# Kernel optimization log

Hardware: AMD Instinct MI355X
Metric: run time of the kernel (lower is better)

## Reference

```python
import jax, jax.numpy as jnp
import numpy as np

B, N = 1, 512
CS, CZ = 384, 128
H, DQK, DV, PQK, PV = 12, 16, 16, 4, 8
EPS = 1e-8
SW = float(np.sqrt(1.0 / (3 * DQK)))            # scalar_weights
PW = float(np.sqrt(1.0 / (3 * PQK * 9.0 / 2)))  # point_weights
ZW = float(np.sqrt(1.0 / 3))                    # attention_2d_weights


def _lin(key, din, dout):
    return 0.02 * jax.random.normal(key, (din, dout), dtype=jnp.float32), jnp.zeros((dout,), dtype=jnp.float32)


def setup_inputs():
    key = jax.random.key(0)
    ks = jax.random.split(key, 16)
    Wsq, bsq = _lin(ks[0], CS, H * DQK)
    Wsk, bsk = _lin(ks[1], CS, H * DQK)
    Wsv, bsv = _lin(ks[2], CS, H * DV)
    Wsb, bsb = _lin(ks[3], CZ, H)
    Wpq, bpq = _lin(ks[4], CS, H * PQK * 3)
    Wpk, bpk = _lin(ks[5], CS, H * PQK * 3)
    Wpv, bpv = _lin(ks[6], CS, H * PV * 3)
    Wout, bout = _lin(ks[7], H * (DV + PV * 4 + CZ), CS)
    w_attn = 0.5 * jax.random.normal(ks[8], (3,), dtype=jnp.float32)  # attn_linear weight (1,3)
    b_attn = jnp.zeros((), dtype=jnp.float32)
    tpw = jnp.full((H,), float(np.log(np.e - 1.0)), dtype=jnp.float32)  # trainable_point_weight
    s = jax.random.normal(ks[9], (B, N, CS), dtype=jnp.float32)
    z = jax.random.normal(ks[10], (B, N, N, CZ), dtype=jnp.float32)
    rot = jax.random.normal(ks[11], (B, N, 3, 3), dtype=jnp.float32)
    tran = jax.random.normal(ks[12], (B, N, 3), dtype=jnp.float32)
    res_mask = jnp.ones((B, N), dtype=jnp.float32)
    return dict(s=s, z=z, rot=rot, tran=tran, res_mask=res_mask,
                Wsq=Wsq, bsq=bsq, Wsk=Wsk, bsk=bsk, Wsv=Wsv, bsv=bsv,
                Wsb=Wsb, bsb=bsb, Wpq=Wpq, bpq=bpq, Wpk=Wpk, bpk=bpk,
                Wpv=Wpv, bpv=bpv, w_attn=w_attn, b_attn=b_attn, tpw=tpw,
                Wout=Wout, bout=bout)


def _ipa(s, z, rot, tran, res_mask, Wsq, bsq, Wsk, bsk, Wsv, bsv, Wsb, bsb,
         Wpq, bpq, Wpk, bpk, Wpv, bpv, w_attn, b_attn, tpw, Wout, bout):
    b, n, _ = s.shape
    sq = (s @ Wsq + bsq).reshape(b, n, H, DQK)
    sk = (s @ Wsk + bsk).reshape(b, n, H, DQK)
    sv = (s @ Wsv + bsv).reshape(b, n, H, DV)
    sb = z @ Wsb + bsb  # [b, i, j, h] pair bias

    def to_global(W, bias, p):
        t = (s @ W + bias).reshape(b, n, H, p, 3)
        return jnp.einsum('bnxy,bnhpy->bnhpx', rot, t) + tran[:, :, None, None, :]

    pqg = to_global(Wpq, bpq, PQK)
    pkg = to_global(Wpk, bpk, PQK)
    pvg = to_global(Wpv, bpv, PV)

    diff = pqg[:, :, None] - pkg[:, None, :]          # [b, i, j, h, p, 3]
    sdist = jnp.sum(diff * diff, axis=(-1, -2))       # [b, i, j, h]

    attn_point = -0.5 * jax.nn.softplus(tpw) * sdist * PW
    attn_scalar = jnp.einsum('bihd,bjhd->bijh', sq * SW, sk)
    attn_pair = sb * ZW
    # attn_linear(stack([scalar, point, pair], -1)).squeeze(-1)
    logits = attn_scalar * w_attn[0] + attn_point * w_attn[1] + attn_pair * w_attn[2] + b_attn

    mask2d = res_mask[:, :, None] * res_mask[:, None, :]
    logits = jnp.where(mask2d[..., None] == 0, jnp.finfo(logits.dtype).min, logits)
    attn = jax.nn.softmax(logits, axis=2)             # softmax over j

    r_scalar = jnp.einsum('bijh,bjhd->bihd', attn, sv)
    r_pt_g = jnp.einsum('bijh,bjhpc->bihpc', attn, pvg)
    # rotate back to local frame: R^T (x - t)
    r_pt = jnp.einsum('biyx,bihpy->bihpx', rot, r_pt_g - tran[:, :, None, None, :])
    r_norm = jnp.sqrt(jnp.sum(r_pt * r_pt, axis=-1) + EPS)  # [b, i, h, p]
    r_pair = jnp.einsum('bijh,bijc->bihc', attn, z)

    cat = jnp.concatenate([r_scalar, r_pt.reshape(b, n, H, PV * 3), r_norm, r_pair], axis=-1)
    return cat.reshape(b, n, -1) @ Wout + bout


def reference(s, z, rot, tran, res_mask, Wsq, bsq, Wsk, bsk, Wsv, bsv, Wsb, bsb,
              Wpq, bpq, Wpk, bpk, Wpv, bpv, w_attn, b_attn, tpw, Wout, bout):
    return _ipa(s, z, rot, tran, res_mask, Wsq, bsq, Wsk, bsk, Wsv, bsv, Wsb, bsb,
                Wpq, bpq, Wpk, bpk, Wpv, bpv, w_attn, b_attn, tpw, Wout, bout)
```

## Files before the change

### kernel.cpp

```cpp
#include <hip/hip_runtime.h>
#include <hip/hip_bf16.h>
#include <math.h>

#define NN 512
#define CSD 384
#define CZ 128
#define HH 12
#define TMPW 1152
#define CATH 176
#define CATDIM 2112
#define NSPLIT 6
#define KSPL 352

#define SW 0.14433756729740643f
#define PW 0.13608276348795434f
#define ZW 0.57735026918962576f
#define NEG_INF -3.4028234663852886e38f

typedef float f32x4_t __attribute__((ext_vector_type(4)));
typedef short bf16x8_t __attribute__((ext_vector_type(8)));

union BFU { uint4 q; bf16x8_t v; ushort u[8]; };

static __device__ __forceinline__ ushort f2bf(float f) {
    __hip_bfloat16 h = __float2bfloat16(f);
    return *reinterpret_cast<ushort*>(&h);
}
static __device__ __forceinline__ float bf2f(ushort u) {
    unsigned int v = ((unsigned int)u) << 16;
    return __uint_as_float(v);
}

__global__ void proj_gemm_kernel(const float* __restrict__ s, const float* __restrict__ rot,
                                 const float* __restrict__ tran,
                                 const float* __restrict__ Wsq, const float* __restrict__ bsq,
                                 const float* __restrict__ Wsk, const float* __restrict__ bsk,
                                 const float* __restrict__ Wsv, const float* __restrict__ bsv,
                                 const float* __restrict__ Wpq, const float* __restrict__ bpq,
                                 const float* __restrict__ Wpk, const float* __restrict__ bpk,
                                 const float* __restrict__ Wpv, const float* __restrict__ bpv,
                                 float* __restrict__ tmp)
{
    int bx = blockIdx.x;
    int n0 = blockIdx.y * 32;
    int f0 = bx * 48;
    const float* W; const float* bb; int dout; int segstart;
    if (bx < 4)       { W = Wsq; bb = bsq; dout = 192; segstart = 0; }
    else if (bx < 8)  { W = Wsk; bb = bsk; dout = 192; segstart = 192; }
    else if (bx < 12) { W = Wsv; bb = bsv; dout = 192; segstart = 384; }
    else if (bx < 15) { W = Wpq; bb = bpq; dout = 144; segstart = 576; }
    else if (bx < 18) { W = Wpk; bb = bpk; dout = 144; segstart = 720; }
    else              { W = Wpv; bb = bpv; dout = 288; segstart = 864; }
    int colbase = f0 - segstart;

    __shared__ float St[32][34];
    __shared__ float Ws[32][49];
    int tid = threadIdx.x;
    int ty = tid >> 4, tx = tid & 15;
    float acc[2][3] = {{0,0,0},{0,0,0}};

    for (int k0 = 0; k0 < CSD; k0 += 32) {
        {
            int r = tid >> 3, c4 = (tid & 7) * 4;
            float4 v = *(const float4*)&s[(size_t)(n0 + r) * CSD + k0 + c4];
            St[c4 + 0][r] = v.x; St[c4 + 1][r] = v.y; St[c4 + 2][r] = v.z; St[c4 + 3][r] = v.w;
        }
        for (int e = tid; e < 1536; e += 256) {
            int r = e / 48, c = e % 48;
            Ws[r][c] = W[(size_t)(k0 + r) * dout + colbase + c];
        }
        __syncthreads();
        #pragma unroll
        for (int k = 0; k < 32; k++) {
            float2 a = *(const float2*)&St[k][ty * 2];
            float b0 = Ws[k][tx * 3], b1 = Ws[k][tx * 3 + 1], b2 = Ws[k][tx * 3 + 2];
            acc[0][0] += a.x * b0; acc[0][1] += a.x * b1; acc[0][2] += a.x * b2;
            acc[1][0] += a.y * b0; acc[1][1] += a.y * b1; acc[1][2] += a.y * b2;
        }
        __syncthreads();
    }
    float bv0 = bb[colbase + tx * 3], bv1 = bb[colbase + tx * 3 + 1], bv2 = bb[colbase + tx * 3 + 2];
    #pragma unroll
    for (int r = 0; r < 2; r++) {
        int n = n0 + ty * 2 + r;
        float v0 = acc[r][0] + bv0, v1 = acc[r][1] + bv1, v2 = acc[r][2] + bv2;
        float* o = tmp + (size_t)n * TMPW + f0 + tx * 3;
        if (bx >= 12) {
            const float* R = rot + n * 9;
            const float* T = tran + n * 3;
            float g0 = R[0] * v0 + R[1] * v1 + R[2] * v2 + T[0];
            float g1 = R[3] * v0 + R[4] * v1 + R[5] * v2 + T[1];
            float g2 = R[6] * v0 + R[7] * v1 + R[8] * v2 + T[2];
            o[0] = g0; o[1] = g1; o[2] = g2;
        } else {
            o[0] = v0; o[1] = v1; o[2] = v2;
        }
    }
}

__global__ void pairbias_mfma_kernel(const float* __restrict__ z, const float* __restrict__ Wsb,
                                     const float* __restrict__ watt, float* __restrict__ sbz)
{
    int tid = threadIdx.x;
    int w = tid >> 6, lane = tid & 63;
    int l16 = lane & 15, lhi = lane >> 4;
    float A2 = watt[2] * ZW;

    BFU breg[4];
    #pragma unroll
    for (int kk = 0; kk < 4; kk++) {
        #pragma unroll
        for (int e = 0; e < 8; e++) {
            int k = kk * 32 + lhi * 8 + e;
            float v = (l16 < HH) ? Wsb[k * HH + l16] * A2 : 0.f;
            breg[kk].u[e] = f2bf(v);
        }
    }

    #pragma unroll
    for (int t = 0; t < 4; t++) {
        size_t r0 = (size_t)blockIdx.x * 256 + (size_t)(t * 4 + w) * 16;
        const float* zrow = z + (r0 + l16) * CZ;
        f32x4_t acc = {0.f, 0.f, 0.f, 0.f};
        #pragma unroll
        for (int kk = 0; kk < 4; kk++) {
            int k0 = kk * 32 + lhi * 8;
            float4 f0 = *(const float4*)&zrow[k0];
            float4 f1 = *(const float4*)&zrow[k0 + 4];
            BFU a;
            a.u[0] = f2bf(f0.x); a.u[1] = f2bf(f0.y); a.u[2] = f2bf(f0.z); a.u[3] = f2bf(f0.w);
            a.u[4] = f2bf(f1.x); a.u[5] = f2bf(f1.y); a.u[6] = f2bf(f1.z); a.u[7] = f2bf(f1.w);
            acc = __builtin_amdgcn_mfma_f32_16x16x32_bf16(a.v, breg[kk].v, acc, 0, 0, 0);
        }
        if (l16 < HH) {
            #pragma unroll
            for (int r = 0; r < 4; r++)
                sbz[(r0 + lhi * 4 + r) * HH + l16] = acc[r];
        }
    }
}

__global__ void logits_softmax_rpair_kernel(const float* __restrict__ z,
                                            const float* __restrict__ sbz,
                                            const float* __restrict__ resm,
                                            const float* __restrict__ bsb,
                                            const float* __restrict__ watt,
                                            const float* __restrict__ batt,
                                            const float* __restrict__ tpw,
                                            const float* __restrict__ tmp,
                                            ushort* __restrict__ attn_bf,
                                            float* __restrict__ cat)
{
    int i = blockIdx.x;
    __shared__ float lt[NN * 17];
    __shared__ uint4 Pl[16 * 64];
    __shared__ float sqs[192];
    __shared__ float pqi[144];
    __shared__ float cpt[12];
    __shared__ float cb[12];
    int tid = threadIdx.x;
    float w0 = watt[0], w1 = watt[1], w2 = watt[2], ba = batt[0];
    float A2 = w2 * ZW;

    for (int k = tid; k < 192; k += 256) sqs[k] = tmp[(size_t)i * TMPW + k] * (SW * w0);
    if (tid < 144) pqi[tid] = tmp[(size_t)i * TMPW + 576 + tid];
    if (tid < 12) {
        cpt[tid] = -0.5f * log1pf(expf(tpw[tid])) * PW * w1;
        cb[tid]  = A2 * bsb[tid] + ba;
    }
    __syncthreads();

    int jg = tid >> 2, hg = tid & 3, h0 = hg * 3;
    float rmi = resm[i];
    const float* sbi = sbz + (size_t)i * NN * HH;

    #pragma unroll
    for (int rr = 0; rr < 8; rr++) {
        int j = jg + 64 * rr;
        float mj = rmi * resm[j];
        const float* sbr = &sbi[(size_t)j * HH + h0];
        float pb[3] = { sbr[0], sbr[1], sbr[2] };
        #pragma unroll
        for (int t = 0; t < 3; t++) {
            int h = h0 + t;
            const float4* skp = (const float4*)(tmp + (size_t)j * TMPW + 192 + h * 16);
            const float4* sqp = (const float4*)&sqs[h * 16];
            float d0 = 0.f;
            #pragma unroll
            for (int q = 0; q < 4; q++) {
                float4 kv = skp[q];
                float4 qv = sqp[q];
                d0 += qv.x * kv.x + qv.y * kv.y + qv.z * kv.z + qv.w * kv.w;
            }
            const float4* pkp = (const float4*)(tmp + (size_t)j * TMPW + 720 + h * 12);
            const float4* pqp = (const float4*)&pqi[h * 12];
            float sd = 0.f;
            #pragma unroll
            for (int q = 0; q < 3; q++) {
                float4 kv = pkp[q];
                float4 qv = pqp[q];
                float a = qv.x - kv.x, bb2 = qv.y - kv.y, cc = qv.z - kv.z, e = qv.w - kv.w;
                sd += a * a + bb2 * bb2 + cc * cc + e * e;
            }
            float lg = cb[h] + pb[t] + d0 + cpt[h] * sd;
            if (mj == 0.f) lg = NEG_INF;
            lt[j * 17 + h] = lg;
        }
    }
    __syncthreads();

    int wid = tid >> 6, lane = tid & 63;
    #pragma unroll
    for (int t = 0; t < 3; t++) {
        int h = wid * 3 + t;
        float v[8]; float m = -INFINITY;
        #pragma unroll
        for (int u = 0; u < 8; u++) { v[u] = lt[(lane + 64 * u) * 17 + h]; m = fmaxf(m, v[u]); }
        for (int off = 32; off; off >>= 1) m = fmaxf(m, __shfl_xor(m, off));
        float ssum = 0.f;
        #pragma unroll
        for (int u = 0; u < 8; u++) { v[u] = __expf(v[u] - m); ssum += v[u]; }
        for (int off = 32; off; off >>= 1) ssum += __shfl_xor(ssum, off);
        float inv = 1.f / ssum;
        #pragma unroll
        for (int u = 0; u < 8; u++) lt[(lane + 64 * u) * 17 + h] = v[u] * inv;
    }
    __syncthreads();

    ushort* ab = attn_bf + (size_t)i * HH * NN;
    #pragma unroll
    for (int u = 0; u < 4; u++) {
        int s2 = tid + 256 * u;
        int m = s2 >> 6, g = s2 & 63;
        BFU val;
        if (m < HH) {
            #pragma unroll
            for (int e = 0; e < 8; e++) val.u[e] = f2bf(lt[(g * 8 + e) * 17 + m]);
            *(uint4*)&ab[(size_t)m * NN + g * 8] = val.q;
        } else {
            val.q.x = 0; val.q.y = 0; val.q.z = 0; val.q.w = 0;
        }
        Pl[m * 64 + (g ^ (m & 7))] = val.q;
    }
    __syncthreads();

    int l16 = lane & 15, lhi = lane >> 4;
    int c0a = (wid * 2 + 0) * 16, c0b = (wid * 2 + 1) * 16;
    f32x4_t acc0 = {0.f, 0.f, 0.f, 0.f};
    f32x4_t acc1 = {0.f, 0.f, 0.f, 0.f};

    for (int kk = 0; kk < 16; kk++) {
        int gidx = kk * 4 + lhi;
        BFU au;
        au.q = Pl[l16 * 64 + (gidx ^ (l16 & 7))];
        const float* zb = z + ((size_t)i * NN + kk * 32 + lhi * 8) * CZ;
        BFU b0, b1;
        #pragma unroll
        for (int e = 0; e < 8; e++) {
            b0.u[e] = f2bf(zb[(size_t)e * CZ + c0a + l16]);
            b1.u[e] = f2bf(zb[(size_t)e * CZ + c0b + l16]);
        }
        acc0 = __builtin_amdgcn_mfma_f32_16x16x32_bf16(au.v, b0.v, acc0, 0, 0, 0);
        acc1 = __builtin_amdgcn_mfma_f32_16x16x32_bf16(au.v, b1.v, acc1, 0, 0, 0);
    }

    #pragma unroll
    for (int r = 0; r < 4; r++) {
        int h = lhi * 4 + r;
        if (h < HH) {
            float* cp = cat + (size_t)i * CATDIM + h * CATH + 48;
            cp[c0a + l16] = acc0[r];
            cp[c0b + l16] = acc1[r];
        }
    }
}

__global__ void head_sum_kernel(const ushort* __restrict__ attn_bf, const float* __restrict__ tmp,
                                const float* __restrict__ rot, const float* __restrict__ tran,
                                float* __restrict__ cat)
{
    int i0 = blockIdx.x * 32;
    int h  = blockIdx.y;
    __shared__ float At[32][65];
    __shared__ float Sr[64][44];
    __shared__ float Rp[32][24];
    int tid = threadIdx.x;
    int il = tid & 31, fg = tid >> 5;
    float acc[5] = {0,0,0,0,0};

    for (int jc = 0; jc < NN; jc += 64) {
        {
            int r = tid >> 3, c8 = (tid & 7) * 8;
            const ushort* src = attn_bf + ((size_t)(i0 + r) * HH + h) * NN + jc + c8;
            BFU v; v.q = *(const uint4*)src;
            #pragma unroll
            for (int q = 0; q < 8; q++) At[r][c8 + q] = bf2f(v.u[q]);
        }
        {
            int jr = tid >> 2, d4 = (tid & 3) * 4;
            *(float4*)&Sr[jr][d4] = *(const float4*)&tmp[(size_t)(jc + jr) * TMPW + 384 + h * 16 + d4];
        }
        for (int e = tid; e < 384; e += 256) {
            int jr = e / 6, p4 = (e % 6) * 4;
            *(float4*)&Sr[jr][16 + p4] = *(const float4*)&tmp[(size_t)(jc + jr) * TMPW + 864 + h * 24 + p4];
        }
        __syncthreads();
        #pragma unroll 4
        for (int j = 0; j < 64; j++) {
            float a = At[il][j];
            #pragma unroll
            for (int q = 0; q < 5; q++) acc[q] += a * Sr[j][fg * 5 + q];
        }
        __syncthreads();
    }

    float* cbase = cat + (size_t)(i0 + il) * CATDIM + h * CATH;
    #pragma unroll
    for (int q = 0; q < 5; q++) {
        int f = fg * 5 + q;
        if (f < 16) cbase[f] = acc[q];
        else Rp[il][f - 16] = acc[q];
    }
    __syncthreads();

    {
        int il2 = tid >> 3, p = tid & 7;
        int i = i0 + il2;
        float gx = Rp[il2][p * 3 + 0] - tran[i * 3 + 0];
        float gy = Rp[il2][p * 3 + 1] - tran[i * 3 + 1];
        float gz = Rp[il2][p * 3 + 2] - tran[i * 3 + 2];
        const float* R = rot + i * 9;
        float lx = R[0] * gx + R[3] * gy + R[6] * gz;
        float ly = R[1] * gx + R[4] * gy + R[7] * gz;
        float lz = R[2] * gx + R[5] * gy + R[8] * gz;
        float nrm = sqrtf(lx * lx + ly * ly + lz * lz + 1e-8f);
        float* cp = cat + (size_t)i * CATDIM + h * CATH;
        cp[16 + p * 3 + 0] = lx; cp[16 + p * 3 + 1] = ly; cp[16 + p * 3 + 2] = lz;
        cp[40 + p] = nrm;
    }
}

__global__ void out_gemm_split_kernel(const float* __restrict__ cat, const float* __restrict__ Wout,
                                      float* __restrict__ part)
{
    int n0 = blockIdx.x * 64;
    int i0 = blockIdx.y * 64;
    int ks = blockIdx.z * KSPL;
    __shared__ float St[32][68];
    __shared__ float Bs[32][68];
    int tid = threadIdx.x;
    int ty = tid >> 4, tx = tid & 15;
    float acc[4][4] = {{0,0,0,0},{0,0,0,0},{0,0,0,0},{0,0,0,0}};

    for (int k0 = 0; k0 < KSPL; k0 += 32) {
        {
            int r = tid >> 2, c8 = (tid & 3) * 8;
            const float* src = cat + (size_t)(i0 + r) * CATDIM + ks + k0 + c8;
            float4 v0 = *(const float4*)src;
            float4 v1 = *(const float4*)(src + 4);
            St[c8+0][r]=v0.x; St[c8+1][r]=v0.y; St[c8+2][r]=v0.z; St[c8+3][r]=v0.w;
            St[c8+4][r]=v1.x; St[c8+5][r]=v1.y; St[c8+6][r]=v1.z; St[c8+7][r]=v1.w;
        }
        {
            int r = tid >> 3, c8 = (tid & 7) * 8;
            const float* src = Wout + (size_t)(ks + k0 + r) * CSD + n0 + c8;
            *(float4*)&Bs[r][c8]     = *(const float4*)src;
            *(float4*)&Bs[r][c8 + 4] = *(const float4*)(src + 4);
        }
        __syncthreads();
        #pragma unroll
        for (int k = 0; k < 32; k++) {
            float4 a = *(const float4*)&St[k][ty * 4];
            float4 b = *(const float4*)&Bs[k][tx * 4];
            float av[4] = {a.x, a.y, a.z, a.w};
            float bv[4] = {b.x, b.y, b.z, b.w};
            #pragma unroll
            for (int r = 0; r < 4; r++)
                #pragma unroll
                for (int c = 0; c < 4; c++) acc[r][c] += av[r] * bv[c];
        }
        __syncthreads();
    }
    #pragma unroll
    for (int r = 0; r < 4; r++) {
        float4 v = make_float4(acc[r][0], acc[r][1], acc[r][2], acc[r][3]);
        *(float4*)&part[((size_t)blockIdx.z * NN + i0 + ty * 4 + r) * CSD + n0 + tx * 4] = v;
    }
}

__global__ void reduce_out_kernel(const float* __restrict__ part, const float* __restrict__ bout,
                                  float* __restrict__ out)
{
    int v = blockIdx.x * 256 + threadIdx.x;
    int n4 = v % 96;
    float4 o = ((const float4*)bout)[n4];
    const float4* p4 = (const float4*)part;
    #pragma unroll
    for (int s = 0; s < NSPLIT; s++) {
        float4 t = p4[(size_t)s * 49152 + v];
        o.x += t.x; o.y += t.y; o.z += t.z; o.w += t.w;
    }
    ((float4*)out)[v] = o;
}

extern "C" void kernel_launch(void* const* d_in, const int* in_sizes, int n_in,
                              void* d_out, int out_size, void* d_ws, size_t ws_size,
                              hipStream_t stream) {
    const float* s    = (const float*)d_in[0];
    const float* z    = (const float*)d_in[1];
    const float* rot  = (const float*)d_in[2];
    const float* tran = (const float*)d_in[3];
    const float* resm = (const float*)d_in[4];
    const float* Wsq  = (const float*)d_in[5];  const float* bsq = (const float*)d_in[6];
    const float* Wsk  = (const float*)d_in[7];  const float* bsk = (const float*)d_in[8];
    const float* Wsv  = (const float*)d_in[9];  const float* bsv = (const float*)d_in[10];
    const float* Wsb  = (const float*)d_in[11]; const float* bsb = (const float*)d_in[12];
    const float* Wpq  = (const float*)d_in[13]; const float* bpq = (const float*)d_in[14];
    const float* Wpk  = (const float*)d_in[15]; const float* bpk = (const float*)d_in[16];
    const float* Wpv  = (const float*)d_in[17]; const float* bpv = (const float*)d_in[18];
    const float* watt = (const float*)d_in[19]; const float* batt = (const float*)d_in[20];
    const float* tpw  = (const float*)d_in[21];
    const float* Wout = (const float*)d_in[22]; const float* bout = (const float*)d_in[23];
    float* out = (float*)d_out;
    float* ws  = (float*)d_ws;

    float* tmp      = ws;
    ushort* attn_bf = (ushort*)(ws + 589824);
    float* sbz      = ws + 589824 + 1572864;
    float* cat      = sbz + 3145728;
    float* partO    = cat + 1081344;

    proj_gemm_kernel<<<dim3(24, 16), 256, 0, stream>>>(s, rot, tran,
                                                       Wsq, bsq, Wsk, bsk, Wsv, bsv,
                                                       Wpq, bpq, Wpk, bpk, Wpv, bpv, tmp);
    pairbias_mfma_kernel<<<1024, 256, 0, stream>>>(z, Wsb, watt, sbz);
    logits_softmax_rpair_kernel<<<512, 256, 0, stream>>>(z, sbz, resm, bsb, watt, batt,
                                                         tpw, tmp, attn_bf, cat);
    head_sum_kernel<<<dim3(16, 12), 256, 0, stream>>>(attn_bf, tmp, rot, tran, cat);
    out_gemm_split_kernel<<<dim3(6, 8, NSPLIT), 256, 0, stream>>>(cat, Wout, partO);
    reduce_out_kernel<<<192, 256, 0, stream>>>(partO, bout, out);
}
```

Baseline: 196.8 us.

## Stage z tiles through LDS transposed in bf16 with register prefetch for r_pair MFMA

The r_pair MFMA used to read z from global memory with strided scalar loads, one element per lane per k-step. It now loads 64-row z chunks with coalesced float4 loads, converts them to bf16, and writes them transposed into a shared zT tile. The next chunk is prefetched into registers while the current one is consumed. MFMA operands are swapped so z is the A operand and attention is B, and the output store is remapped to match. This costs extra LDS, which may lower occupancy, plus two barriers per chunk.

```diff
diff --git a/kernel.cpp b/kernel.cpp
--- a/kernel.cpp
+++ b/kernel.cpp
@@ -154,6 +154,7 @@
     int i = blockIdx.x;
     __shared__ float lt[NN * 17];
     __shared__ uint4 Pl[16 * 64];
+    __shared__ ushort zT[128 * 72];
     __shared__ float sqs[192];
     __shared__ float pqi[144];
     __shared__ float cpt[12];
@@ -242,35 +243,54 @@
         }
         Pl[m * 64 + (g ^ (m & 7))] = val.q;
     }
-    __syncthreads();
 
     int l16 = lane & 15, lhi = lane >> 4;
-    int c0a = (wid * 2 + 0) * 16, c0b = (wid * 2 + 1) * 16;
+    int mt0 = wid * 2;
     f32x4_t acc0 = {0.f, 0.f, 0.f, 0.f};
     f32x4_t acc1 = {0.f, 0.f, 0.f, 0.f};
-
-    for (int kk = 0; kk < 16; kk++) {
-        int gidx = kk * 4 + lhi;
-        BFU au;
-        au.q = Pl[l16 * 64 + (gidx ^ (l16 & 7))];
-        const float* zb = z + ((size_t)i * NN + kk * 32 + lhi * 8) * CZ;
-        BFU b0, b1;
-        #pragma unroll
-        for (int e = 0; e < 8; e++) {
-            b0.u[e] = f2bf(zb[(size_t)e * CZ + c0a + l16]);
-            b1.u[e] = f2bf(zb[(size_t)e * CZ + c0b + l16]);
-        }
-        acc0 = __builtin_amdgcn_mfma_f32_16x16x32_bf16(au.v, b0.v, acc0, 0, 0, 0);
-        acc1 = __builtin_amdgcn_mfma_f32_16x16x32_bf16(au.v, b1.v, acc1, 0, 0, 0);
-    }
-
-    #pragma unroll
-    for (int r = 0; r < 4; r++) {
-        int h = lhi * 4 + r;
-        if (h < HH) {
-            float* cp = cat + (size_t)i * CATDIM + h * CATH + 48;
-            cp[c0a + l16] = acc0[r];
-            cp[c0b + l16] = acc1[r];
+    int jrow = tid >> 2, cq = tid & 3;
+    const float* zsl = z + (size_t)i * NN * CZ;
+    float4 pr[8];
+    {
+        const float* zr0 = zsl + (size_t)jrow * CZ;
+        #pragma unroll
+        for (int q = 0; q < 8; q++) pr[q] = *(const float4*)&zr0[cq * 4 + q * 16];
+    }
+    for (int jc = 0; jc < 8; jc++) {
+        __syncthreads();
+        #pragma unroll
+        for (int q = 0; q < 8; q++) {
+            float4 v = pr[q];
+            int cb2 = cq * 4 + q * 16;
+            zT[(cb2 + 0) * 72 + jrow] = f2bf(v.x);
+            zT[(cb2 + 1) * 72 + jrow] = f2bf(v.y);
+            zT[(cb2 + 2) * 72 + jrow] = f2bf(v.z);
+            zT[(cb2 + 3) * 72 + jrow] = f2bf(v.w);
+        }
+        if (jc < 7) {
+            const float* zr1 = zsl + (size_t)((jc + 1) * 64 + jrow) * CZ;
+            #pragma unroll
+            for (int q = 0; q < 8; q++) pr[q] = *(const float4*)&zr1[cq * 4 + q * 16];
+        }
+        __syncthreads();
+        #pragma unroll
+        for (int kkl = 0; kkl < 2; kkl++) {
+            int g = jc * 8 + kkl * 4 + lhi;
+            BFU bfrag; bfrag.q = Pl[l16 * 64 + (g ^ (l16 & 7))];
+            int jl = kkl * 32 + lhi * 8;
+            BFU a0, a1;
+            a0.q = *(const uint4*)&zT[(mt0 * 16 + l16) * 72 + jl];
+            a1.q = *(const uint4*)&zT[((mt0 + 1) * 16 + l16) * 72 + jl];
+            acc0 = __builtin_amdgcn_mfma_f32_16x16x32_bf16(a0.v, bfrag.v, acc0, 0, 0, 0);
+            acc1 = __builtin_amdgcn_mfma_f32_16x16x32_bf16(a1.v, bfrag.v, acc1, 0, 0, 0);
+        }
+    }
+    if (l16 < HH) {
+        float* cp = cat + (size_t)i * CATDIM + l16 * CATH + 48;
+        #pragma unroll
+        for (int r = 0; r < 4; r++) {
+            cp[mt0 * 16 + lhi * 4 + r]       = acc0[r];
+            cp[(mt0 + 1) * 16 + lhi * 4 + r] = acc1[r];
         }
     }
 }
```

Result: no change. 193.8 us (-1.5%).

## Fuse pair-bias projection into logits/softmax/r_pair kernel with 512 threads

Applied to the files above, without the earlier changes.

Merges the pair-bias MFMA kernel into the per-row logits, softmax and r_pair kernel, so each block computes the bias for row i from z into shared memory instead of writing and reading a global sbz buffer. The z row is read twice within one block, so the second pass may hit in cache rather than requiring a separate kernel's full z sweep. The r_pair contraction switches from bf16 MFMA to fp32 FMA over four j-quarter slabs that are reduced through shared memory. Blocks grow to 512 threads with larger shared-memory use, which may reduce occupancy, and the fp32 r_pair path does more ALU work.

```diff
diff --git a/kernel.cpp b/kernel.cpp
--- a/kernel.cpp
+++ b/kernel.cpp
@@ -98,180 +98,179 @@
     }
 }
 
-__global__ void pairbias_mfma_kernel(const float* __restrict__ z, const float* __restrict__ Wsb,
-                                     const float* __restrict__ watt, float* __restrict__ sbz)
-{
-    int tid = threadIdx.x;
-    int w = tid >> 6, lane = tid & 63;
-    int l16 = lane & 15, lhi = lane >> 4;
-    float A2 = watt[2] * ZW;
-
-    BFU breg[4];
-    #pragma unroll
-    for (int kk = 0; kk < 4; kk++) {
-        #pragma unroll
-        for (int e = 0; e < 8; e++) {
-            int k = kk * 32 + lhi * 8 + e;
-            float v = (l16 < HH) ? Wsb[k * HH + l16] * A2 : 0.f;
-            breg[kk].u[e] = f2bf(v);
-        }
-    }
-
-    #pragma unroll
-    for (int t = 0; t < 4; t++) {
-        size_t r0 = (size_t)blockIdx.x * 256 + (size_t)(t * 4 + w) * 16;
-        const float* zrow = z + (r0 + l16) * CZ;
-        f32x4_t acc = {0.f, 0.f, 0.f, 0.f};
-        #pragma unroll
-        for (int kk = 0; kk < 4; kk++) {
-            int k0 = kk * 32 + lhi * 8;
-            float4 f0 = *(const float4*)&zrow[k0];
-            float4 f1 = *(const float4*)&zrow[k0 + 4];
-            BFU a;
-            a.u[0] = f2bf(f0.x); a.u[1] = f2bf(f0.y); a.u[2] = f2bf(f0.z); a.u[3] = f2bf(f0.w);
-            a.u[4] = f2bf(f1.x); a.u[5] = f2bf(f1.y); a.u[6] = f2bf(f1.z); a.u[7] = f2bf(f1.w);
-            acc = __builtin_amdgcn_mfma_f32_16x16x32_bf16(a.v, breg[kk].v, acc, 0, 0, 0);
-        }
-        if (l16 < HH) {
-            #pragma unroll
-            for (int r = 0; r < 4; r++)
-                sbz[(r0 + lhi * 4 + r) * HH + l16] = acc[r];
-        }
-    }
-}
-
-__global__ void logits_softmax_rpair_kernel(const float* __restrict__ z,
-                                            const float* __restrict__ sbz,
-                                            const float* __restrict__ resm,
-                                            const float* __restrict__ bsb,
-                                            const float* __restrict__ watt,
-                                            const float* __restrict__ batt,
-                                            const float* __restrict__ tpw,
-                                            const float* __restrict__ tmp,
-                                            ushort* __restrict__ attn_bf,
-                                            float* __restrict__ cat)
+__global__ __launch_bounds__(512) void fused_z_kernel(const float* __restrict__ z,
+                                                      const float* __restrict__ resm,
+                                                      const float* __restrict__ Wsb,
+                                                      const float* __restrict__ bsb,
+                                                      const float* __restrict__ watt,
+                                                      const float* __restrict__ batt,
+                                                      const float* __restrict__ tpw,
+                                                      const float* __restrict__ tmp,
+                                                      ushort* __restrict__ attn_bf,
+                                                      float* __restrict__ cat)
 {
     int i = blockIdx.x;
     __shared__ float lt[NN * 17];
-    __shared__ uint4 Pl[16 * 64];
+    __shared__ float sbz[NN * 12];
     __shared__ float sqs[192];
     __shared__ float pqi[144];
     __shared__ float cpt[12];
     __shared__ float cb[12];
     int tid = threadIdx.x;
+    int w = tid >> 6, lane = tid & 63;
+    int l16 = lane & 15, lhi = lane >> 4;
     float w0 = watt[0], w1 = watt[1], w2 = watt[2], ba = batt[0];
     float A2 = w2 * ZW;
 
-    for (int k = tid; k < 192; k += 256) sqs[k] = tmp[(size_t)i * TMPW + k] * (SW * w0);
+    for (int k = tid; k < 192; k += 512) sqs[k] = tmp[(size_t)i * TMPW + k] * (SW * w0);
     if (tid < 144) pqi[tid] = tmp[(size_t)i * TMPW + 576 + tid];
     if (tid < 12) {
         cpt[tid] = -0.5f * log1pf(expf(tpw[tid])) * PW * w1;
         cb[tid]  = A2 * bsb[tid] + ba;
     }
+
+    BFU breg[4];
+    #pragma unroll
+    for (int kk = 0; kk < 4; kk++) {
+        #pragma unroll
+        for (int e = 0; e < 8; e++) {
+            int k = kk * 32 + lhi * 8 + e;
+            float v = (l16 < HH) ? Wsb[k * HH + l16] * A2 : 0.f;
+            breg[kk].u[e] = f2bf(v);
+        }
+    }
+
+    const float* zi = z + (size_t)i * NN * CZ;
+    float4 prA[8], prB[8];
+    {
+        const float* zr = zi + (size_t)(w * 16 + l16) * CZ + lhi * 8;
+        #pragma unroll
+        for (int kk = 0; kk < 4; kk++) {
+            prA[kk * 2]     = *(const float4*)&zr[kk * 32];
+            prA[kk * 2 + 1] = *(const float4*)&zr[kk * 32 + 4];
+        }
+    }
+    #pragma unroll
+    for (int t = 0; t < 4; t++) {
+        float4* cur = (t & 1) ? prB : prA;
+        float4* nxt = (t & 1) ? prA : prB;
+        if (t < 3) {
+            const float* zr = zi + (size_t)((w + 8 * (t + 1)) * 16 + l16) * CZ + lhi * 8;
+            #pragma unroll
+            for (int kk = 0; kk < 4; kk++) {
+                nxt[kk * 2]     = *(const float4*)&zr[kk * 32];
+                nxt[kk * 2 + 1] = *(const float4*)&zr[kk * 32 + 4];
+            }
+        }
+        f32x4_t acc = {0.f, 0.f, 0.f, 0.f};
+        #pragma unroll
+        for (int kk = 0; kk < 4; kk++) {
+            float4 f0 = cur[kk * 2], f1 = cur[kk * 2 + 1];
+            BFU a;
+            a.u[0] = f2bf(f0.x); a.u[1] = f2bf(f0.y); a.u[2] = f2bf(f0.z); a.u[3] = f2bf(f0.w);
+            a.u[4] = f2bf(f1.x); a.u[5] = f2bf(f1.y); a.u[6] = f2bf(f1.z); a.u[7] = f2bf(f1.w);
+            acc = __builtin_amdgcn_mfma_f32_16x16x32_bf16(a.v, breg[kk].v, acc, 0, 0, 0);
+        }
+        if (l16 < HH) {
+            int T = w + 8 * t;
+            #pragma unroll
+            for (int r = 0; r < 4; r++)
+                sbz[(T * 16 + lhi * 4 + r) * 12 + l16] = acc[r];
+        }
+    }
     __syncthreads();
 
-    int jg = tid >> 2, hg = tid & 3, h0 = hg * 3;
-    float rmi = resm[i];
-    const float* sbi = sbz + (size_t)i * NN * HH;
-
-    #pragma unroll
-    for (int rr = 0; rr < 8; rr++) {
-        int j = jg + 64 * rr;
-        float mj = rmi * resm[j];
-        const float* sbr = &sbi[(size_t)j * HH + h0];
-        float pb[3] = { sbr[0], sbr[1], sbr[2] };
+    {
+        int jg = tid >> 2, hg = tid & 3, h0 = hg * 3;
+        float rmi = resm[i];
+        #pragma unroll
+        for (int rr = 0; rr < 4; rr++) {
+            int j = jg + 128 * rr;
+            float mj = rmi * resm[j];
+            const float* sbr = &sbz[j * 12 + h0];
+            #pragma unroll
+            for (int t = 0; t < 3; t++) {
+                int h = h0 + t;
+                const float4* skp = (const float4*)(tmp + (size_t)j * TMPW + 192 + h * 16);
+                const float4* sqp = (const float4*)&sqs[h * 16];
+                float d0 = 0.f;
+                #pragma unroll
+                for (int q = 0; q < 4; q++) {
+                    float4 kv = skp[q];
+                    float4 qv = sqp[q];
+                    d0 += qv.x * kv.x + qv.y * kv.y + qv.z * kv.z + qv.w * kv.w;
+                }
+                const float4* pkp = (const float4*)(tmp + (size_t)j * TMPW + 720 + h * 12);
+                const float4* pqp = (const float4*)&pqi[h * 12];
+                float sd = 0.f;
+                #pragma unroll
+                for (int q = 0; q < 3; q++) {
+                    float4 kv = pkp[q];
+                    float4 qv = pqp[q];
+                    float a = qv.x - kv.x, bb2 = qv.y - kv.y, cc = qv.z - kv.z, e = qv.w - kv.w;
+                    sd += a * a + bb2 * bb2 + cc * cc + e * e;
+                }
+                float lg = cb[h] + sbr[t] + d0 + cpt[h] * sd;
+                if (mj == 0.f) lg = NEG_INF;
+                lt[j * 17 + h] = lg;
+            }
+        }
+    }
+    __syncthreads();
+
+    if (w < 4) {
         #pragma unroll
         for (int t = 0; t < 3; t++) {
-            int h = h0 + t;
-            const float4* skp = (const float4*)(tmp + (size_t)j * TMPW + 192 + h * 16);
-            const float4* sqp = (const float4*)&sqs[h * 16];
-            float d0 = 0.f;
-            #pragma unroll
-            for (int q = 0; q < 4; q++) {
-                float4 kv = skp[q];
-                float4 qv = sqp[q];
-                d0 += qv.x * kv.x + qv.y * kv.y + qv.z * kv.z + qv.w * kv.w;
+            int h = w * 3 + t;
+            float v[8]; float m = -INFINITY;
+            #pragma unroll
+            for (int u = 0; u < 8; u++) { v[u] = lt[(lane + 64 * u) * 17 + h]; m = fmaxf(m, v[u]); }
+            for (int off = 32; off; off >>= 1) m = fmaxf(m, __shfl_xor(m, off));
+            float ssum = 0.f;
+            #pragma unroll
+            for (int u = 0; u < 8; u++) { v[u] = __expf(v[u] - m); ssum += v[u]; }
+            for (int off = 32; off; off >>= 1) ssum += __shfl_xor(ssum, off);
+            float inv = 1.f / ssum;
+            ushort* ag = attn_bf + ((size_t)i * HH + h) * NN;
+            #pragma unroll
+            for (int u = 0; u < 8; u++) {
+                float p = v[u] * inv;
+                lt[(lane + 64 * u) * 17 + h] = p;
+                ag[lane + 64 * u] = f2bf(p);
             }
-            const float4* pkp = (const float4*)(tmp + (size_t)j * TMPW + 720 + h * 12);
-            const float4* pqp = (const float4*)&pqi[h * 12];
-            float sd = 0.f;
-            #pragma unroll
-            for (int q = 0; q < 3; q++) {
-                float4 kv = pkp[q];
-                float4 qv = pqp[q];
-                float a = qv.x - kv.x, bb2 = qv.y - kv.y, cc = qv.z - kv.z, e = qv.w - kv.w;
-                sd += a * a + bb2 * bb2 + cc * cc + e * e;
+        }
+    }
+    __syncthreads();
+
+    {
+        int jq = w >> 1;
+        int c = (w & 1) * 64 + lane;
+        float acc[12];
+        #pragma unroll
+        for (int h = 0; h < 12; h++) acc[h] = 0.f;
+        const float* zq = zi + (size_t)(jq * 128) * CZ + c;
+        for (int j = 0; j < 128; j += 8) {
+            float zv[8];
+            #pragma unroll
+            for (int u = 0; u < 8; u++) zv[u] = zq[(size_t)(j + u) * CZ];
+            #pragma unroll
+            for (int u = 0; u < 8; u++) {
+                const float* pr = &lt[(jq * 128 + j + u) * 17];
+                #pragma unroll
+                for (int h = 0; h < 12; h++) acc[h] += pr[h] * zv[u];
             }
-            float lg = cb[h] + pb[t] + d0 + cpt[h] * sd;
-            if (mj == 0.f) lg = NEG_INF;
-            lt[j * 17 + h] = lg;
-        }
+        }
+        float* pslab = sbz;
+        #pragma unroll
+        for (int h = 0; h < 12; h++) pslab[(jq * 12 + h) * 128 + c] = acc[h];
     }
     __syncthreads();
 
-    int wid = tid >> 6, lane = tid & 63;
-    #pragma unroll
-    for (int t = 0; t < 3; t++) {
-        int h = wid * 3 + t;
-        float v[8]; float m = -INFINITY;
-        #pragma unroll
-        for (int u = 0; u < 8; u++) { v[u] = lt[(lane + 64 * u) * 17 + h]; m = fmaxf(m, v[u]); }
-        for (int off = 32; off; off >>= 1) m = fmaxf(m, __shfl_xor(m, off));
-        float ssum = 0.f;
-        #pragma unroll
-        for (int u = 0; u < 8; u++) { v[u] = __expf(v[u] - m); ssum += v[u]; }
-        for (int off = 32; off; off >>= 1) ssum += __shfl_xor(ssum, off);
-        float inv = 1.f / ssum;
-        #pragma unroll
-        for (int u = 0; u < 8; u++) lt[(lane + 64 * u) * 17 + h] = v[u] * inv;
-    }
-    __syncthreads();
-
-    ushort* ab = attn_bf + (size_t)i * HH * NN;
-    #pragma unroll
-    for (int u = 0; u < 4; u++) {
-        int s2 = tid + 256 * u;
-        int m = s2 >> 6, g = s2 & 63;
-        BFU val;
-        if (m < HH) {
-            #pragma unroll
-            for (int e = 0; e < 8; e++) val.u[e] = f2bf(lt[(g * 8 + e) * 17 + m]);
-            *(uint4*)&ab[(size_t)m * NN + g * 8] = val.q;
-        } else {
-            val.q.x = 0; val.q.y = 0; val.q.z = 0; val.q.w = 0;
-        }
-        Pl[m * 64 + (g ^ (m & 7))] = val.q;
-    }
-    __syncthreads();
-
-    int l16 = lane & 15, lhi = lane >> 4;
-    int c0a = (wid * 2 + 0) * 16, c0b = (wid * 2 + 1) * 16;
-    f32x4_t acc0 = {0.f, 0.f, 0.f, 0.f};
-    f32x4_t acc1 = {0.f, 0.f, 0.f, 0.f};
-
-    for (int kk = 0; kk < 16; kk++) {
-        int gidx = kk * 4 + lhi;
-        BFU au;
-        au.q = Pl[l16 * 64 + (gidx ^ (l16 & 7))];
-        const float* zb = z + ((size_t)i * NN + kk * 32 + lhi * 8) * CZ;
-        BFU b0, b1;
-        #pragma unroll
-        for (int e = 0; e < 8; e++) {
-            b0.u[e] = f2bf(zb[(size_t)e * CZ + c0a + l16]);
-            b1.u[e] = f2bf(zb[(size_t)e * CZ + c0b + l16]);
-        }
-        acc0 = __builtin_amdgcn_mfma_f32_16x16x32_bf16(au.v, b0.v, acc0, 0, 0, 0);
-        acc1 = __builtin_amdgcn_mfma_f32_16x16x32_bf16(au.v, b1.v, acc1, 0, 0, 0);
-    }
-
-    #pragma unroll
-    for (int r = 0; r < 4; r++) {
-        int h = lhi * 4 + r;
-        if (h < HH) {
-            float* cp = cat + (size_t)i * CATDIM + h * CATH + 48;
-            cp[c0a + l16] = acc0[r];
-            cp[c0b + l16] = acc1[r];
-        }
+    for (int e = tid; e < 1536; e += 512) {
+        int h = e >> 7, c = e & 127;
+        float ssum = sbz[h * 128 + c] + sbz[(12 + h) * 128 + c]
+                   + sbz[(24 + h) * 128 + c] + sbz[(36 + h) * 128 + c];
+        cat[(size_t)i * CATDIM + h * CATH + 48 + c] = ssum;
     }
 }
 
@@ -424,18 +423,16 @@
     float* out = (float*)d_out;
     float* ws  = (float*)d_ws;
 
-    float* tmp      = ws;
+    float*  tmp     = ws;
     ushort* attn_bf = (ushort*)(ws + 589824);
-    float* sbz      = ws + 589824 + 1572864;
-    float* cat      = sbz + 3145728;
-    float* partO    = cat + 1081344;
+    float*  cat     = ws + 589824 + 1572864;
+    float*  partO   = cat + 1081344;
 
     proj_gemm_kernel<<<dim3(24, 16), 256, 0, stream>>>(s, rot, tran,
                                                        Wsq, bsq, Wsk, bsk, Wsv, bsv,
                                                        Wpq, bpq, Wpk, bpk, Wpv, bpv, tmp);
-    pairbias_mfma_kernel<<<1024, 256, 0, stream>>>(z, Wsb, watt, sbz);
-    logits_softmax_rpair_kernel<<<512, 256, 0, stream>>>(z, sbz, resm, bsb, watt, batt,
-                                                         tpw, tmp, attn_bf, cat);
+    fused_z_kernel<<<512, 512, 0, stream>>>(z, resm, Wsb, bsb, watt, batt, tpw,
+                                            tmp, attn_bf, cat);
     head_sum_kernel<<<dim3(16, 12), 256, 0, stream>>>(attn_bf, tmp, rot, tran, cat);
     out_gemm_split_kernel<<<dim3(6, 8, NSPLIT), 256, 0, stream>>>(cat, Wout, partO);
     reduce_out_kernel<<<192, 256, 0, stream>>>(partO, bout, out);
```

After: 182.3 us. -7.4%, faster.
